# Kernel tuning notes

Measured on AMD Instinct MI355X. Metric: run time of the kernel, lower is better.

The kernel has to match this reference:

```python
import jax, jax.numpy as jnp
import numpy as np

N = 24  # input_size
TRIL = N * (N + 1) // 2  # 300
_rows, _cols = np.tril_indices(N)  # row-major order, matches torch.tril_indices


def setup_inputs() -> dict:
    key = jax.random.key(0)
    ks = jax.random.split(key, 8)
    B = 131072
    x = jax.random.normal(ks[0], (B, N), dtype=jnp.float32)
    # MLP params: Linear(N,128), Linear(128,32), Linear(32,TRIL)
    def lin(k, fan_in, fan_out):
        k1, k2 = jax.random.split(k)
        lim = 1.0 / np.sqrt(fan_in)
        W = jax.random.uniform(k1, (fan_out, fan_in), jnp.float32, -lim, lim)
        b = jax.random.uniform(k2, (fan_out,), jnp.float32, -lim, lim)
        return W, b
    W1, b1 = lin(ks[1], N, 128)
    W2, b2 = lin(ks[2], 128, 32)
    W3, b3 = lin(ks[3], 32, TRIL)
    return {"x": x, "W1": W1, "b1": b1, "W2": W2, "b2": b2, "W3": W3, "b3": b3}


def reference(x, W1, b1, W2, b2, W3, b3):
    # MLP: Linear -> ELU -> Linear -> ELU -> Linear -> Softplus
    h = jax.nn.elu(x @ W1.T + b1)           # [B,128]
    h = jax.nn.elu(h @ W2.T + b2)           # [B,32]
    c = jax.nn.softplus(h @ W3.T + b3)      # [B,TRIL]
    B = x.shape[0]
    # scatter into lower-triangular Cholesky factor
    L = jnp.zeros((B, N, N), dtype=x.dtype).at[:, _rows, _cols].set(c)  # [B,N,N]
    A = jnp.einsum('bij,bkj->bik', L, L)    # C @ C^T, SPD
    y = jnp.einsum('bi,bij,bj->b', x, A, x)[:, None]  # quadratic form, [B,1]
    return y
```

## Files before the change

kernel.cpp:

```cpp
#include <hip/hip_runtime.h>
#include <hip/hip_bf16.h>
#include <math.h>


constexpr int NI  = 24;
constexpr int H1  = 128;
constexpr int H2  = 32;
constexpr int SPB = 128;
constexpr int NT_TOT = 19;
constexpr int W3R = 304;
constexpr float LOG2E = 1.4426950408889634f;
constexpr float LN2SQ = 0.4804530139182014f;

typedef __attribute__((ext_vector_type(8))) short bf16x8;
typedef __attribute__((ext_vector_type(4))) float f32x4;

struct TriMap { unsigned char i[320]; unsigned char j[320]; };
constexpr TriMap mk_map() {
    TriMap m{};
    int t = 0;
    for (int i = 0; i < NI; ++i)
        for (int j = 0; j <= i; ++j) { m.i[t] = (unsigned char)i; m.j[t] = (unsigned char)j; ++t; }
    for (; t < 320; ++t) { m.i[t] = 0; m.j[t] = 0; }
    return m;
}
constexpr TriMap TM = mk_map();

__device__ __forceinline__ float elu_f(float v) {
    return v > 0.0f ? v : __expf(v) - 1.0f;
}
__device__ __forceinline__ float exp2_hw(float x) {
    float r; asm("v_exp_f32 %0, %1" : "=v"(r) : "v"(x)); return r;
}
__device__ __forceinline__ float log2_hw(float x) {
    float r; asm("v_log_f32 %0, %1" : "=v"(r) : "v"(x)); return r;
}
__device__ __forceinline__ float softplus_g(float zp) {
    return fmaxf(zp, 0.0f) + log2_hw(1.0f + exp2_hw(-fabsf(zp)));
}
__device__ __forceinline__ unsigned short f2bf(float f) {
    return __builtin_bit_cast(unsigned short, __float2bfloat16(f));
}
__device__ __forceinline__ unsigned int pk2(float a, float b) {
    return (unsigned int)f2bf(a) | ((unsigned int)f2bf(b) << 16);
}

__global__ void wcvt(const float* __restrict__ W1, const float* __restrict__ W2,
                     const float* __restrict__ W3, const float* __restrict__ b3,
                     unsigned short* __restrict__ ws) {
    int idx = blockIdx.x * 256 + threadIdx.x;
    if (idx < 4096) {
        int n = idx >> 5, k = idx & 31;
        ws[idx] = f2bf(k < NI ? W1[n * NI + k] : 0.0f);
    } else if (idx < 8192) {
        ws[idx] = f2bf(W2[idx - 4096]);
    } else if (idx < 8192 + W3R * H2) {
        int j = idx - 8192;
        int t = j >> 5;
        ws[idx] = f2bf(t < 300 ? W3[j] * LOG2E : 0.0f);
    } else if (idx < 8192 + W3R * H2 + W3R) {
        int t = idx - (8192 + W3R * H2);
        float* b3s = reinterpret_cast<float*>(ws + 17920);
        b3s[t] = (t < 300) ? b3[t] * LOG2E : 0.0f;
    }
}

template<int CH, int HF>
__device__ __forceinline__ void consume3(const float* __restrict__ crow,
                                         const float xr[NI], float v[NI]) {
    constexpr int T0 = CH * 32 + HF * 16;
    if constexpr (T0 < 300) {
        const f32x4* p = reinterpret_cast<const f32x4*>(crow + HF * 16);
        f32x4 cc[4];
        cc[0] = p[0]; cc[1] = p[1]; cc[2] = p[2]; cc[3] = p[3];
        #pragma unroll
        for (int tl = 0; tl < 16; ++tl) {
            if (T0 + tl < 300)
                v[TM.j[T0 + tl]] =
                    fmaf(xr[TM.i[T0 + tl]], cc[tl >> 2][tl & 3], v[TM.j[T0 + tl]]);
        }
    }
}

template<int CH>
__device__ __forceinline__ void chunk3(
    int w_hi, int w_lo, int lr, int lq, int sid, int half,
    const unsigned short* __restrict__ w3b, const float* __restrict__ b3s,
    const float xr[NI], float v[NI],
    float* __restrict__ c_buf, const unsigned short* __restrict__ h2b)
{
    const int my_nt = 2 * CH + w_hi;
    if (my_nt < NT_TOT) {
        const int trow = my_nt * 16;
        bf16x8 af = *reinterpret_cast<const bf16x8*>(w3b + (trow + lr) * H2 + lq * 8);
        const float4 b4 = *reinterpret_cast<const float4*>(b3s + trow + 4 * lq);
        #pragma unroll
        for (int q = 0; q < 4; ++q) {
            const int st = 4 * w_lo + q;
            bf16x8 hb = *reinterpret_cast<const bf16x8*>(h2b + (st * 16 + lr) * 40 + lq * 8);
            f32x4 a = {0.f, 0.f, 0.f, 0.f};
            a = __builtin_amdgcn_mfma_f32_16x16x32_bf16(af, hb, a, 0, 0, 0);
            f32x4 w;
            w[0] = softplus_g(a[0] + b4.x);
            w[1] = softplus_g(a[1] + b4.y);
            w[2] = softplus_g(a[2] + b4.z);
            w[3] = softplus_g(a[3] + b4.w);
            *reinterpret_cast<f32x4*>(
                c_buf + (st * 16 + lr) * 36 + (my_nt & 1) * 16 + 4 * lq) = w;
        }
    }
    __syncthreads();
    if (half == 0) consume3<CH, 0>(c_buf + sid * 36, xr, v);
    else           consume3<CH, 1>(c_buf + sid * 36, xr, v);
    __syncthreads();
}

__global__ __launch_bounds__(256, 4) void qnet_fused(
    const float* __restrict__ x,
    const unsigned short* __restrict__ w1b, const float* __restrict__ b1,
    const unsigned short* __restrict__ w2b, const float* __restrict__ b2,
    const unsigned short* __restrict__ w3b, const float* __restrict__ b3s,
    float* __restrict__ y, int B)
{
    __shared__ __align__(16) unsigned char L[30720];
    unsigned short* xb  = reinterpret_cast<unsigned short*>(L);
    unsigned short* h1s = reinterpret_cast<unsigned short*>(L + 10240);
    unsigned short* h2b = reinterpret_cast<unsigned short*>(L + 20480);
    float* c_buf = reinterpret_cast<float*>(L);

    const int tid  = threadIdx.x;
    const int sid  = tid & (SPB - 1);
    const int lane = tid & 63;
    const int lr   = lane & 15, lq = lane >> 4;
    const int half = __builtin_amdgcn_readfirstlane(tid >> 7);
    const int wid  = __builtin_amdgcn_readfirstlane(tid >> 6);
    const int w_hi = wid >> 1, w_lo = wid & 1;
    const size_t sbase = (size_t)blockIdx.x * SPB;

    float xr[NI];
    {
        const float4* xp4 = reinterpret_cast<const float4*>(x + (sbase + sid) * NI);
        #pragma unroll
        for (int q = 0; q < NI / 4; ++q) {
            float4 t4 = xp4[q];
            xr[4*q+0] = t4.x; xr[4*q+1] = t4.y; xr[4*q+2] = t4.z; xr[4*q+3] = t4.w;
        }
    }
    if (half == 0) {
        unsigned int pk[12];
        #pragma unroll
        for (int q = 0; q < 12; ++q) pk[q] = pk2(xr[2*q], xr[2*q+1]);
        uint4* dst = reinterpret_cast<uint4*>(xb + sid * 40);
        dst[0] = make_uint4(pk[0], pk[1], pk[2], pk[3]);
        dst[1] = make_uint4(pk[4], pk[5], pk[6], pk[7]);
        dst[2] = make_uint4(pk[8], pk[9], pk[10], pk[11]);
    } else {
        *reinterpret_cast<uint4*>(xb + sid * 40 + 24) = make_uint4(0, 0, 0, 0);
    }
    __syncthreads();

    f32x4 acc[2][2];
    #pragma unroll
    for (int u = 0; u < 2; ++u)
        #pragma unroll
        for (int n2 = 0; n2 < 2; ++n2) acc[u][n2] = (f32x4){0.f, 0.f, 0.f, 0.f};

    #pragma unroll
    for (int kk = 0; kk < 4; ++kk) {
        const int nt1 = 2 * kk + w_hi;
        bf16x8 af = *reinterpret_cast<const bf16x8*>(w1b + (nt1 * 16 + lr) * 32 + lq * 8);
        const float4 bb1 = *reinterpret_cast<const float4*>(b1 + nt1 * 16 + 4 * lq);
        #pragma unroll
        for (int q = 0; q < 4; ++q) {
            const int st = 4 * w_lo + q;
            bf16x8 bf = *reinterpret_cast<const bf16x8*>(xb + (st * 16 + lr) * 40 + lq * 8);
            f32x4 a = {0.f, 0.f, 0.f, 0.f};
            a = __builtin_amdgcn_mfma_f32_16x16x32_bf16(af, bf, a, 0, 0, 0);
            unsigned int p0 = pk2(elu_f(a[0] + bb1.x), elu_f(a[1] + bb1.y));
            unsigned int p1 = pk2(elu_f(a[2] + bb1.z), elu_f(a[3] + bb1.w));
            unsigned long long pw = (unsigned long long)p0 | ((unsigned long long)p1 << 32);
            *reinterpret_cast<unsigned long long*>(
                h1s + (st * 16 + lr) * 40 + w_hi * 16 + 4 * lq) = pw;
        }
        __syncthreads();
        #pragma unroll
        for (int u = 0; u < 2; ++u) {
            const int st2 = 2 * wid + u;
            bf16x8 hb = *reinterpret_cast<const bf16x8*>(h1s + (st2 * 16 + lr) * 40 + lq * 8);
            #pragma unroll
            for (int n2 = 0; n2 < 2; ++n2) {
                bf16x8 wf = *reinterpret_cast<const bf16x8*>(
                    w2b + (n2 * 16 + lr) * H1 + kk * 32 + lq * 8);
                acc[u][n2] = __builtin_amdgcn_mfma_f32_16x16x32_bf16(wf, hb, acc[u][n2], 0, 0, 0);
            }
        }
        __syncthreads();
    }

    #pragma unroll
    for (int u = 0; u < 2; ++u) {
        const int st2 = 2 * wid + u;
        #pragma unroll
        for (int n2 = 0; n2 < 2; ++n2) {
            const float4 bb2 = *reinterpret_cast<const float4*>(b2 + n2 * 16 + 4 * lq);
            unsigned int p0 = pk2(elu_f(acc[u][n2][0] + bb2.x), elu_f(acc[u][n2][1] + bb2.y));
            unsigned int p1 = pk2(elu_f(acc[u][n2][2] + bb2.z), elu_f(acc[u][n2][3] + bb2.w));
            unsigned long long pw = (unsigned long long)p0 | ((unsigned long long)p1 << 32);
            *reinterpret_cast<unsigned long long*>(
                h2b + (st2 * 16 + lr) * 40 + n2 * 16 + 4 * lq) = pw;
        }
    }
    __syncthreads();

    float v[NI];
    #pragma unroll
    for (int q = 0; q < NI; ++q) v[q] = 0.f;

    chunk3<0>(w_hi, w_lo, lr, lq, sid, half, w3b, b3s, xr, v, c_buf, h2b);
    chunk3<1>(w_hi, w_lo, lr, lq, sid, half, w3b, b3s, xr, v, c_buf, h2b);
    chunk3<2>(w_hi, w_lo, lr, lq, sid, half, w3b, b3s, xr, v, c_buf, h2b);
    chunk3<3>(w_hi, w_lo, lr, lq, sid, half, w3b, b3s, xr, v, c_buf, h2b);
    chunk3<4>(w_hi, w_lo, lr, lq, sid, half, w3b, b3s, xr, v, c_buf, h2b);
    chunk3<5>(w_hi, w_lo, lr, lq, sid, half, w3b, b3s, xr, v, c_buf, h2b);
    chunk3<6>(w_hi, w_lo, lr, lq, sid, half, w3b, b3s, xr, v, c_buf, h2b);
    chunk3<7>(w_hi, w_lo, lr, lq, sid, half, w3b, b3s, xr, v, c_buf, h2b);
    chunk3<8>(w_hi, w_lo, lr, lq, sid, half, w3b, b3s, xr, v, c_buf, h2b);
    chunk3<9>(w_hi, w_lo, lr, lq, sid, half, w3b, b3s, xr, v, c_buf, h2b);

    float* vx = c_buf;
    if (half == 1) {
        f32x4* dst = reinterpret_cast<f32x4*>(vx + sid * 24);
        #pragma unroll
        for (int q = 0; q < 6; ++q) {
            f32x4 t4 = { v[4*q], v[4*q+1], v[4*q+2], v[4*q+3] };
            dst[q] = t4;
        }
    }
    __syncthreads();
    if (half == 0) {
        const f32x4* src = reinterpret_cast<const f32x4*>(vx + sid * 24);
        float acc_y = 0.f;
        #pragma unroll
        for (int q = 0; q < 6; ++q) {
            f32x4 t4 = src[q];
            #pragma unroll
            for (int r = 0; r < 4; ++r) {
                float sv = v[4*q + r] + t4[r];
                acc_y = fmaf(sv, sv, acc_y);
            }
        }
        y[sbase + sid] = LN2SQ * acc_y;
    }
}

extern "C" void kernel_launch(void* const* d_in, const int* in_sizes, int n_in,
                              void* d_out, int out_size, void* d_ws, size_t ws_size,
                              hipStream_t stream) {
    const float* x  = (const float*)d_in[0];
    const float* W1 = (const float*)d_in[1];
    const float* b1 = (const float*)d_in[2];
    const float* W2 = (const float*)d_in[3];
    const float* b2 = (const float*)d_in[4];
    const float* W3 = (const float*)d_in[5];
    const float* b3 = (const float*)d_in[6];
    float* y = (float*)d_out;

    unsigned short* ws = (unsigned short*)d_ws;
    const unsigned short* w1b = ws;
    const unsigned short* w2b = ws + 4096;
    const unsigned short* w3b = ws + 8192;
    const float* b3s = reinterpret_cast<const float*>(ws + 17920);

    const int B = in_sizes[0] / NI;
    const int cvt_elems = 8192 + W3R * H2 + W3R;
    wcvt<<<dim3((cvt_elems + 255) / 256), dim3(256), 0, stream>>>(W1, W2, W3, b3, ws);
    qnet_fused<<<dim3(B / SPB), dim3(256), 0, stream>>>(
        x, w1b, b1, w2b, b2, w3b, b3s, y, B);
}
```

Measured before the change: 38.70 us.

## Shrink block to two waves owning sample tiles, dropping most barriers

The block now processes 64 samples with 128 threads. Each wave owns its own sample tiles through layers 1 and 2 and loads x directly into MFMA operand registers, so the x staging buffer in LDS goes away. In layer 3 each wave writes and then consumes only its own column half of the c buffer, which removes the two barriers per layer-2 step and per layer-3 chunk. The cost is that each wave now recomputes all layer-1 output tiles for its own samples, and blocks are smaller with more of them. Padding the K dimension relies on the zero-padded W1 columns, because lanes with lq==3 reload real x values.

```diff
diff --git a/kernel.cpp b/kernel.cpp
--- a/kernel.cpp
+++ b/kernel.cpp
@@ -6,7 +6,7 @@
 constexpr int NI  = 24;
 constexpr int H1  = 128;
 constexpr int H2  = 32;
-constexpr int SPB = 128;
+constexpr int SPB = 64;
 constexpr int NT_TOT = 19;
 constexpr int W3R = 304;
 constexpr float LOG2E = 1.4426950408889634f;
@@ -84,19 +84,17 @@
 
 template<int CH>
 __device__ __forceinline__ void chunk3(
-    int w_hi, int w_lo, int lr, int lq, int sid, int half,
+    int half, int lr, int lq, int lane,
     const unsigned short* __restrict__ w3b, const float* __restrict__ b3s,
     const float xr[NI], float v[NI],
     float* __restrict__ c_buf, const unsigned short* __restrict__ h2b)
 {
-    const int my_nt = 2 * CH + w_hi;
+    const int my_nt = 2 * CH + half;
     if (my_nt < NT_TOT) {
-        const int trow = my_nt * 16;
-        bf16x8 af = *reinterpret_cast<const bf16x8*>(w3b + (trow + lr) * H2 + lq * 8);
-        const float4 b4 = *reinterpret_cast<const float4*>(b3s + trow + 4 * lq);
-        #pragma unroll
-        for (int q = 0; q < 4; ++q) {
-            const int st = 4 * w_lo + q;
+        bf16x8 af = *reinterpret_cast<const bf16x8*>(w3b + (my_nt * 16 + lr) * H2 + lq * 8);
+        const float4 b4 = *reinterpret_cast<const float4*>(b3s + my_nt * 16 + 4 * lq);
+        #pragma unroll
+        for (int st = 0; st < 4; ++st) {
             bf16x8 hb = *reinterpret_cast<const bf16x8*>(h2b + (st * 16 + lr) * 40 + lq * 8);
             f32x4 a = {0.f, 0.f, 0.f, 0.f};
             a = __builtin_amdgcn_mfma_f32_16x16x32_bf16(af, hb, a, 0, 0, 0);
@@ -106,58 +104,56 @@
             w[2] = softplus_g(a[2] + b4.z);
             w[3] = softplus_g(a[3] + b4.w);
             *reinterpret_cast<f32x4*>(
-                c_buf + (st * 16 + lr) * 36 + (my_nt & 1) * 16 + 4 * lq) = w;
-        }
-    }
-    __syncthreads();
-    if (half == 0) consume3<CH, 0>(c_buf + sid * 36, xr, v);
-    else           consume3<CH, 1>(c_buf + sid * 36, xr, v);
-    __syncthreads();
-}
-
-__global__ __launch_bounds__(256, 4) void qnet_fused(
+                c_buf + (st * 16 + lr) * 36 + half * 16 + 4 * lq) = w;
+        }
+    }
+    if (half == 0) consume3<CH, 0>(c_buf + lane * 36, xr, v);
+    else           consume3<CH, 1>(c_buf + lane * 36, xr, v);
+}
+
+__global__ __launch_bounds__(128, 4) void qnet_fused(
     const float* __restrict__ x,
     const unsigned short* __restrict__ w1b, const float* __restrict__ b1,
     const unsigned short* __restrict__ w2b, const float* __restrict__ b2,
     const unsigned short* __restrict__ w3b, const float* __restrict__ b3s,
     float* __restrict__ y, int B)
 {
-    __shared__ __align__(16) unsigned char L[30720];
-    unsigned short* xb  = reinterpret_cast<unsigned short*>(L);
-    unsigned short* h1s = reinterpret_cast<unsigned short*>(L + 10240);
-    unsigned short* h2b = reinterpret_cast<unsigned short*>(L + 20480);
+    __shared__ __align__(16) unsigned char L[14336];
+    unsigned short* h1s = reinterpret_cast<unsigned short*>(L);
+    unsigned short* h2b = reinterpret_cast<unsigned short*>(L + 9216);
     float* c_buf = reinterpret_cast<float*>(L);
+    float* vx    = reinterpret_cast<float*>(L);
 
     const int tid  = threadIdx.x;
-    const int sid  = tid & (SPB - 1);
     const int lane = tid & 63;
     const int lr   = lane & 15, lq = lane >> 4;
-    const int half = __builtin_amdgcn_readfirstlane(tid >> 7);
-    const int wid  = __builtin_amdgcn_readfirstlane(tid >> 6);
-    const int w_hi = wid >> 1, w_lo = wid & 1;
+    const int half = __builtin_amdgcn_readfirstlane(tid >> 6);
     const size_t sbase = (size_t)blockIdx.x * SPB;
 
     float xr[NI];
     {
-        const float4* xp4 = reinterpret_cast<const float4*>(x + (sbase + sid) * NI);
+        const float4* xp4 = reinterpret_cast<const float4*>(x + (sbase + lane) * NI);
         #pragma unroll
         for (int q = 0; q < NI / 4; ++q) {
             float4 t4 = xp4[q];
             xr[4*q+0] = t4.x; xr[4*q+1] = t4.y; xr[4*q+2] = t4.z; xr[4*q+3] = t4.w;
         }
     }
-    if (half == 0) {
-        unsigned int pk[12];
-        #pragma unroll
-        for (int q = 0; q < 12; ++q) pk[q] = pk2(xr[2*q], xr[2*q+1]);
-        uint4* dst = reinterpret_cast<uint4*>(xb + sid * 40);
-        dst[0] = make_uint4(pk[0], pk[1], pk[2], pk[3]);
-        dst[1] = make_uint4(pk[4], pk[5], pk[6], pk[7]);
-        dst[2] = make_uint4(pk[8], pk[9], pk[10], pk[11]);
-    } else {
-        *reinterpret_cast<uint4*>(xb + sid * 40 + 24) = make_uint4(0, 0, 0, 0);
-    }
-    __syncthreads();
+
+    bf16x8 xf[2];
+    #pragma unroll
+    for (int u = 0; u < 2; ++u) {
+        const int st = 2 * half + u;
+        const float* xp = x + (sbase + st * 16 + lr) * NI + (lq == 3 ? 0 : lq * 8);
+        float4 x0 = *reinterpret_cast<const float4*>(xp);
+        float4 x1 = *reinterpret_cast<const float4*>(xp + 4);
+        bf16x8 bf;
+        bf[0] = (short)f2bf(x0.x); bf[1] = (short)f2bf(x0.y);
+        bf[2] = (short)f2bf(x0.z); bf[3] = (short)f2bf(x0.w);
+        bf[4] = (short)f2bf(x1.x); bf[5] = (short)f2bf(x1.y);
+        bf[6] = (short)f2bf(x1.z); bf[7] = (short)f2bf(x1.w);
+        xf[u] = bf;
+    }
 
     f32x4 acc[2][2];
     #pragma unroll
@@ -167,25 +163,26 @@
 
     #pragma unroll
     for (int kk = 0; kk < 4; ++kk) {
-        const int nt1 = 2 * kk + w_hi;
-        bf16x8 af = *reinterpret_cast<const bf16x8*>(w1b + (nt1 * 16 + lr) * 32 + lq * 8);
-        const float4 bb1 = *reinterpret_cast<const float4*>(b1 + nt1 * 16 + 4 * lq);
-        #pragma unroll
-        for (int q = 0; q < 4; ++q) {
-            const int st = 4 * w_lo + q;
-            bf16x8 bf = *reinterpret_cast<const bf16x8*>(xb + (st * 16 + lr) * 40 + lq * 8);
-            f32x4 a = {0.f, 0.f, 0.f, 0.f};
-            a = __builtin_amdgcn_mfma_f32_16x16x32_bf16(af, bf, a, 0, 0, 0);
-            unsigned int p0 = pk2(elu_f(a[0] + bb1.x), elu_f(a[1] + bb1.y));
-            unsigned int p1 = pk2(elu_f(a[2] + bb1.z), elu_f(a[3] + bb1.w));
-            unsigned long long pw = (unsigned long long)p0 | ((unsigned long long)p1 << 32);
-            *reinterpret_cast<unsigned long long*>(
-                h1s + (st * 16 + lr) * 40 + w_hi * 16 + 4 * lq) = pw;
-        }
-        __syncthreads();
+        #pragma unroll
+        for (int n = 0; n < 2; ++n) {
+            const int nt1 = 2 * kk + n;
+            bf16x8 af = *reinterpret_cast<const bf16x8*>(w1b + (nt1 * 16 + lr) * 32 + lq * 8);
+            const float4 bb1 = *reinterpret_cast<const float4*>(b1 + nt1 * 16 + 4 * lq);
+            #pragma unroll
+            for (int u = 0; u < 2; ++u) {
+                const int st = 2 * half + u;
+                f32x4 a = {0.f, 0.f, 0.f, 0.f};
+                a = __builtin_amdgcn_mfma_f32_16x16x32_bf16(af, xf[u], a, 0, 0, 0);
+                unsigned int p0 = pk2(elu_f(a[0] + bb1.x), elu_f(a[1] + bb1.y));
+                unsigned int p1 = pk2(elu_f(a[2] + bb1.z), elu_f(a[3] + bb1.w));
+                unsigned long long pw = (unsigned long long)p0 | ((unsigned long long)p1 << 32);
+                *reinterpret_cast<unsigned long long*>(
+                    h1s + (st * 16 + lr) * 40 + n * 16 + 4 * lq) = pw;
+            }
+        }
         #pragma unroll
         for (int u = 0; u < 2; ++u) {
-            const int st2 = 2 * wid + u;
+            const int st2 = 2 * half + u;
             bf16x8 hb = *reinterpret_cast<const bf16x8*>(h1s + (st2 * 16 + lr) * 40 + lq * 8);
             #pragma unroll
             for (int n2 = 0; n2 < 2; ++n2) {
@@ -194,12 +191,11 @@
                 acc[u][n2] = __builtin_amdgcn_mfma_f32_16x16x32_bf16(wf, hb, acc[u][n2], 0, 0, 0);
             }
         }
-        __syncthreads();
     }
 
     #pragma unroll
     for (int u = 0; u < 2; ++u) {
-        const int st2 = 2 * wid + u;
+        const int st2 = 2 * half + u;
         #pragma unroll
         for (int n2 = 0; n2 < 2; ++n2) {
             const float4 bb2 = *reinterpret_cast<const float4*>(b2 + n2 * 16 + 4 * lq);
@@ -216,20 +212,20 @@
     #pragma unroll
     for (int q = 0; q < NI; ++q) v[q] = 0.f;
 
-    chunk3<0>(w_hi, w_lo, lr, lq, sid, half, w3b, b3s, xr, v, c_buf, h2b);
-    chunk3<1>(w_hi, w_lo, lr, lq, sid, half, w3b, b3s, xr, v, c_buf, h2b);
-    chunk3<2>(w_hi, w_lo, lr, lq, sid, half, w3b, b3s, xr, v, c_buf, h2b);
-    chunk3<3>(w_hi, w_lo, lr, lq, sid, half, w3b, b3s, xr, v, c_buf, h2b);
-    chunk3<4>(w_hi, w_lo, lr, lq, sid, half, w3b, b3s, xr, v, c_buf, h2b);
-    chunk3<5>(w_hi, w_lo, lr, lq, sid, half, w3b, b3s, xr, v, c_buf, h2b);
-    chunk3<6>(w_hi, w_lo, lr, lq, sid, half, w3b, b3s, xr, v, c_buf, h2b);
-    chunk3<7>(w_hi, w_lo, lr, lq, sid, half, w3b, b3s, xr, v, c_buf, h2b);
-    chunk3<8>(w_hi, w_lo, lr, lq, sid, half, w3b, b3s, xr, v, c_buf, h2b);
-    chunk3<9>(w_hi, w_lo, lr, lq, sid, half, w3b, b3s, xr, v, c_buf, h2b);
-
-    float* vx = c_buf;
+    chunk3<0>(half, lr, lq, lane, w3b, b3s, xr, v, c_buf, h2b);
+    chunk3<1>(half, lr, lq, lane, w3b, b3s, xr, v, c_buf, h2b);
+    chunk3<2>(half, lr, lq, lane, w3b, b3s, xr, v, c_buf, h2b);
+    chunk3<3>(half, lr, lq, lane, w3b, b3s, xr, v, c_buf, h2b);
+    chunk3<4>(half, lr, lq, lane, w3b, b3s, xr, v, c_buf, h2b);
+    chunk3<5>(half, lr, lq, lane, w3b, b3s, xr, v, c_buf, h2b);
+    chunk3<6>(half, lr, lq, lane, w3b, b3s, xr, v, c_buf, h2b);
+    chunk3<7>(half, lr, lq, lane, w3b, b3s, xr, v, c_buf, h2b);
+    chunk3<8>(half, lr, lq, lane, w3b, b3s, xr, v, c_buf, h2b);
+    chunk3<9>(half, lr, lq, lane, w3b, b3s, xr, v, c_buf, h2b);
+
+    __syncthreads();
     if (half == 1) {
-        f32x4* dst = reinterpret_cast<f32x4*>(vx + sid * 24);
+        f32x4* dst = reinterpret_cast<f32x4*>(vx + lane * 24);
         #pragma unroll
         for (int q = 0; q < 6; ++q) {
             f32x4 t4 = { v[4*q], v[4*q+1], v[4*q+2], v[4*q+3] };
@@ -238,7 +234,7 @@
     }
     __syncthreads();
     if (half == 0) {
-        const f32x4* src = reinterpret_cast<const f32x4*>(vx + sid * 24);
+        const f32x4* src = reinterpret_cast<const f32x4*>(vx + lane * 24);
         float acc_y = 0.f;
         #pragma unroll
         for (int q = 0; q < 6; ++q) {
@@ -249,7 +245,7 @@
                 acc_y = fmaf(sv, sv, acc_y);
             }
         }
-        y[sbase + sid] = LN2SQ * acc_y;
+        y[sbase + lane] = LN2SQ * acc_y;
     }
 }
 
@@ -274,6 +270,6 @@
     const int B = in_sizes[0] / NI;
     const int cvt_elems = 8192 + W3R * H2 + W3R;
     wcvt<<<dim3((cvt_elems + 255) / 256), dim3(256), 0, stream>>>(W1, W2, W3, b3, ws);
-    qnet_fused<<<dim3(B / SPB), dim3(256), 0, stream>>>(
+    qnet_fused<<<dim3(B / SPB), dim3(128), 0, stream>>>(
         x, w1b, b1, w2b, b2, w3b, b3s, y, B);
 }
```

Measured after the change: 37.51 us. 1.03x faster.
